# Optimization experiments

Hardware: AMD Instinct MI355X
Metric: run time of the kernel (lower is better)

The kernel has to match this reference:

```python
import jax, jax.numpy as jnp
import numpy as np

N_NODES = 200000
FEAT_DIM = 256
EMB_DIM = 64
N_EXP = 100000
N_TARGETS = 1024
MAX_CAND = 128


def setup_inputs() -> dict:
    key = jax.random.key(0)
    ks = jax.random.split(key, 10)
    return {
        "x": jax.random.normal(ks[0], (N_NODES, FEAT_DIM), jnp.float32),
        "h": jax.random.normal(ks[1], (N_NODES, EMB_DIM), jnp.float32),
        "degree": jax.random.uniform(ks[2], (N_NODES,), jnp.float32),
        "beta": jax.random.uniform(ks[3], (N_NODES,), jnp.float32),
        "exp_nodes": jax.random.randint(ks[4], (N_EXP,), 0, N_NODES),
        "idx_targets": jax.random.randint(ks[5], (N_TARGETS,), 0, N_NODES),
        "W_raw": jax.random.normal(ks[6], (FEAT_DIM, EMB_DIM), jnp.float32) / np.float32(np.sqrt(FEAT_DIM)),
        "b_raw": jnp.zeros((EMB_DIM,), jnp.float32),
        "W_num": jax.random.normal(ks[7], (2, EMB_DIM), jnp.float32),
        "b_num": jnp.zeros((EMB_DIM,), jnp.float32),
        "W1": jax.random.normal(ks[8], (4 * EMB_DIM, EMB_DIM), jnp.float32) / np.float32(np.sqrt(4 * EMB_DIM)),
        "b1": jnp.zeros((EMB_DIM,), jnp.float32),
        "W2": jax.random.normal(ks[9], (EMB_DIM, 1), jnp.float32) / np.float32(np.sqrt(EMB_DIM)),
        "b2": jnp.zeros((1,), jnp.float32),
        "temperature": jnp.float32(1.0),
        "epsilon": jnp.float32(1.0),
    }


def reference(x, h, degree, beta, exp_nodes, idx_targets,
              W_raw, b_raw, W_num, b_num, W1, b1, W2, b2,
              temperature, epsilon):
    # gather node features and project (irregular gather + small GEMM)
    x_v = x[exp_nodes] @ W_raw + b_raw                       # [E, emb]
    h_v = h[exp_nodes]                                       # [E, emb]
    h_T = jnp.broadcast_to(h[idx_targets].mean(axis=0)[None, :],
                           (exp_nodes.shape[0], EMB_DIM))    # [E, emb]
    numerics = jnp.stack([degree[exp_nodes], beta[exp_nodes]], axis=-1)  # [E, 2]
    emb_num = numerics @ W_num + b_num                       # [E, emb]
    emb = jax.nn.relu(jnp.concatenate([x_v, h_v, h_T, emb_num], axis=-1))  # [E, 4*emb]
    # dropout is identity in eval mode
    hidden = jax.nn.relu(emb @ W1 + b1)                      # [E, emb]
    scores = (hidden @ W2 + b2)[:, 0]                        # [E]
    # straight-through gumbel top-k (eval: no gumbel noise, epsilon unused)
    y = jax.nn.softmax(scores / temperature)
    _, idx = jax.lax.top_k(y, MAX_CAND)
    y_hard = jnp.zeros_like(y).at[idx].set(1.0)
    y_st = jax.lax.stop_gradient(y_hard - y) + y
    candidates = y_st[idx]                                   # [MAX_CAND] (== 1.0 fwd)
    cand_indices = exp_nodes[idx]                            # [MAX_CAND]
    return candidates, cand_indices
```

## Files before the change

kernel.cpp:

```cpp
#include <hip/hip_runtime.h>
#include <stdint.h>

#define RELU(v) ((v) > 0.0f ? (v) : 0.0f)

typedef unsigned long long u64;
typedef unsigned int u32;
typedef unsigned short u16;
typedef float f32x4 __attribute__((ext_vector_type(4)));
typedef short bf16x8 __attribute__((ext_vector_type(8)));

constexpr int FEAT = 256;
constexpr int EMB  = 64;

constexpr int STG_ROW = 264;
constexpr int WAVE_BYTES = 16 * STG_ROW * 2;
constexpr int XV_ROW = 68;

__device__ inline u16 bf16_trunc(float v) { return (u16)(__float_as_uint(v) >> 16); }

__device__ inline u32 score_key(float s) {
    u32 u = __float_as_uint(s);
    return (u & 0x80000000u) ? ~u : (u | 0x80000000u);
}

__device__ inline bf16x8 pack_bf16x8(float4 lo, float4 hi) {
    bf16x8 r;
    r[0] = (short)bf16_trunc(lo.x); r[1] = (short)bf16_trunc(lo.y);
    r[2] = (short)bf16_trunc(lo.z); r[3] = (short)bf16_trunc(lo.w);
    r[4] = (short)bf16_trunc(hi.x); r[5] = (short)bf16_trunc(hi.y);
    r[6] = (short)bf16_trunc(hi.z); r[7] = (short)bf16_trunc(hi.w);
    return r;
}

__global__ __launch_bounds__(1024) void setup_kernel(
    const float* __restrict__ h, const int* __restrict__ idx_targets, int nT,
    const float* __restrict__ W_raw, const float* __restrict__ W1, const float* __restrict__ b1,
    float* __restrict__ bias_eff, u16* __restrict__ wrawpk, u16* __restrict__ w1pk)
{
    const int tid = threadIdx.x;
    if (blockIdx.x == 1) {
        for (int t = tid; t < 2048; t += 1024) {
            int ks   = t >> 8;
            int c    = (t >> 6) & 3;
            int lane = t & 63;
            int n    = c * 16 + (lane & 15);
            int kbase = ks * 32 + ((lane >> 4) << 3);
            #pragma unroll
            for (int j = 0; j < 8; ++j) {
                int k = kbase + j;
                wrawpk[t * 8 + j] = bf16_trunc(W_raw[(size_t)k * EMB + n]);
                w1pk  [t * 8 + j] = bf16_trunc(W1   [(size_t)k * EMB + n]);
            }
        }
        return;
    }
    __shared__ int   idx_s[1024];
    __shared__ float partial[16][64];
    __shared__ float hT[64];
    const int nid = nT > 1024 ? 1024 : nT;
    for (int i = tid; i < nid; i += 1024) idx_s[i] = idx_targets[i];
    __syncthreads();
    const int d = tid & 63, grp = tid >> 6;
    float s = 0.f;
    for (int t = grp; t < nid; t += 16)
        s += h[(size_t)idx_s[t] * EMB + d];
    partial[grp][d] = s;
    __syncthreads();
    if (tid < 64) {
        float m = 0.f;
        #pragma unroll
        for (int g = 0; g < 16; ++g) m += partial[g][tid];
        hT[tid] = RELU(m / (float)nT);
    }
    __syncthreads();
    if (tid < 64) {
        float acc = b1[tid];
        #pragma unroll 8
        for (int dd = 0; dd < 64; ++dd)
            acc = fmaf(hT[dd], W1[(size_t)(128 + dd) * EMB + tid], acc);
        bias_eff[tid] = acc;
    }
}

__global__ __launch_bounds__(256) void approx_score_kernel(
    const float* __restrict__ x, const float* __restrict__ h,
    const float* __restrict__ degree, const float* __restrict__ beta,
    const int* __restrict__ exp_nodes,
    const u16* __restrict__ wrawpk, const u16* __restrict__ w1pk,
    const float* __restrict__ b_raw,
    const float* __restrict__ W_num, const float* __restrict__ b_num,
    const float* __restrict__ W2, const float* __restrict__ bias_eff,
    u64* __restrict__ pairs, int E)
{
    __shared__ __align__(16) unsigned char smem[4][WAVE_BYTES];

    const int tid  = threadIdx.x;
    const int wid  = tid >> 6;
    const int lane = tid & 63;
    const int rloc = lane & 15;
    const int kgrp = lane >> 4;
    const int koff = kgrp * 8;
    const int tileBase = blockIdx.x * 64;

    const int grow = tileBase + wid * 16 + rloc;
    const int node = exp_nodes[grow < E ? grow : 0];
    const float* hrow = h + (size_t)node * EMB;
    const float dg = degree[node];
    const float bt = beta[node];

    u16*   stg = (u16*)&smem[wid][0];
    float* xvp = (float*)&smem[wid][0];

    #pragma unroll
    for (int half = 0; half < 2; ++half) {
        float4 v0, v1, v2, v3, v4, v5, v6, v7;
        {
            int r = half * 8;
            v0 = *reinterpret_cast<const float4*>(x + (size_t)__shfl(node, r + 0) * FEAT + lane * 4);
            v1 = *reinterpret_cast<const float4*>(x + (size_t)__shfl(node, r + 1) * FEAT + lane * 4);
            v2 = *reinterpret_cast<const float4*>(x + (size_t)__shfl(node, r + 2) * FEAT + lane * 4);
            v3 = *reinterpret_cast<const float4*>(x + (size_t)__shfl(node, r + 3) * FEAT + lane * 4);
            v4 = *reinterpret_cast<const float4*>(x + (size_t)__shfl(node, r + 4) * FEAT + lane * 4);
            v5 = *reinterpret_cast<const float4*>(x + (size_t)__shfl(node, r + 5) * FEAT + lane * 4);
            v6 = *reinterpret_cast<const float4*>(x + (size_t)__shfl(node, r + 6) * FEAT + lane * 4);
            v7 = *reinterpret_cast<const float4*>(x + (size_t)__shfl(node, r + 7) * FEAT + lane * 4);
        }
        #define STG_WRITE(rr, vv) { \
            ushort4 pk; pk.x = bf16_trunc(vv.x); pk.y = bf16_trunc(vv.y); \
            pk.z = bf16_trunc(vv.z); pk.w = bf16_trunc(vv.w); \
            *reinterpret_cast<ushort4*>(stg + (half * 8 + rr) * STG_ROW + lane * 4) = pk; }
        STG_WRITE(0, v0) STG_WRITE(1, v1) STG_WRITE(2, v2) STG_WRITE(3, v3)
        STG_WRITE(4, v4) STG_WRITE(5, v5) STG_WRITE(6, v6) STG_WRITE(7, v7)
        #undef STG_WRITE
    }
    __builtin_amdgcn_wave_barrier();

    f32x4 acc1[4];
    #pragma unroll
    for (int c = 0; c < 4; ++c) {
        float bv = b_raw[c * 16 + rloc];
        acc1[c] = (f32x4){bv, bv, bv, bv};
    }
    #pragma unroll
    for (int ks = 0; ks < 8; ++ks) {
        bf16x8 a = *reinterpret_cast<const bf16x8*>(stg + rloc * STG_ROW + ks * 32 + koff);
        #pragma unroll
        for (int c = 0; c < 4; ++c) {
            bf16x8 b = *reinterpret_cast<const bf16x8*>(wrawpk + (size_t)((ks * 4 + c) * 64 + lane) * 8);
            acc1[c] = __builtin_amdgcn_mfma_f32_16x16x32_bf16(a, b, acc1[c], 0, 0, 0);
        }
    }
    __builtin_amdgcn_wave_barrier();

    #pragma unroll
    for (int c = 0; c < 4; ++c)
        #pragma unroll
        for (int r = 0; r < 4; ++r)
            xvp[(kgrp * 4 + r) * XV_ROW + c * 16 + rloc] = RELU(acc1[c][r]);
    __builtin_amdgcn_wave_barrier();

    f32x4 acc2[4];
    #pragma unroll
    for (int c = 0; c < 4; ++c) {
        float bv = bias_eff[c * 16 + rloc];
        acc2[c] = (f32x4){bv, bv, bv, bv};
    }

    #pragma unroll
    for (int ks = 0; ks < 2; ++ks) {
        float4 lo = *reinterpret_cast<const float4*>(hrow + ks * 32 + koff);
        float4 hi = *reinterpret_cast<const float4*>(hrow + ks * 32 + koff + 4);
        lo.x = RELU(lo.x); lo.y = RELU(lo.y); lo.z = RELU(lo.z); lo.w = RELU(lo.w);
        hi.x = RELU(hi.x); hi.y = RELU(hi.y); hi.z = RELU(hi.z); hi.w = RELU(hi.w);
        bf16x8 a = pack_bf16x8(lo, hi);
        #pragma unroll
        for (int c = 0; c < 4; ++c) {
            bf16x8 b = *reinterpret_cast<const bf16x8*>(w1pk + (size_t)(((2 + ks) * 4 + c) * 64 + lane) * 8);
            acc2[c] = __builtin_amdgcn_mfma_f32_16x16x32_bf16(a, b, acc2[c], 0, 0, 0);
        }
    }

    #pragma unroll
    for (int ks = 0; ks < 2; ++ks) {
        bf16x8 a;
        #pragma unroll
        for (int j = 0; j < 8; ++j) {
            int k = ks * 32 + koff + j;
            float v = RELU(fmaf(dg, W_num[k], fmaf(bt, W_num[EMB + k], b_num[k])));
            a[j] = (short)bf16_trunc(v);
        }
        #pragma unroll
        for (int c = 0; c < 4; ++c) {
            bf16x8 b = *reinterpret_cast<const bf16x8*>(w1pk + (size_t)(((6 + ks) * 4 + c) * 64 + lane) * 8);
            acc2[c] = __builtin_amdgcn_mfma_f32_16x16x32_bf16(a, b, acc2[c], 0, 0, 0);
        }
    }

    #pragma unroll
    for (int ks = 0; ks < 2; ++ks) {
        float4 lo = *reinterpret_cast<const float4*>(xvp + rloc * XV_ROW + ks * 32 + koff);
        float4 hi = *reinterpret_cast<const float4*>(xvp + rloc * XV_ROW + ks * 32 + koff + 4);
        bf16x8 a = pack_bf16x8(lo, hi);
        #pragma unroll
        for (int c = 0; c < 4; ++c) {
            bf16x8 b = *reinterpret_cast<const bf16x8*>(w1pk + (size_t)((ks * 4 + c) * 64 + lane) * 8);
            acc2[c] = __builtin_amdgcn_mfma_f32_16x16x32_bf16(a, b, acc2[c], 0, 0, 0);
        }
    }

    float p[4] = {0.f, 0.f, 0.f, 0.f};
    #pragma unroll
    for (int c = 0; c < 4; ++c) {
        float w2v = W2[c * 16 + rloc];
        #pragma unroll
        for (int r = 0; r < 4; ++r)
            p[r] = fmaf(RELU(acc2[c][r]), w2v, p[r]);
    }
    #pragma unroll
    for (int m = 1; m < 16; m <<= 1) {
        p[0] += __shfl_xor(p[0], m);
        p[1] += __shfl_xor(p[1], m);
        p[2] += __shfl_xor(p[2], m);
        p[3] += __shfl_xor(p[3], m);
    }
    if (rloc == 0) {
        #pragma unroll
        for (int r = 0; r < 4; ++r) {
            int g = tileBase + wid * 16 + kgrp * 4 + r;
            if (g < E)
                pairs[g] = ((u64)score_key(p[r]) << 32) | (u32)(~(u32)g);
        }
    }
}

template<int N, int NT>
__device__ inline void bitonic_desc(u64* s, int tid) {
    for (int k = 2; k <= N; k <<= 1) {
        for (int j = k >> 1; j > 0; j >>= 1) {
            __syncthreads();
            for (int i = tid; i < N; i += NT) {
                int ixj = i ^ j;
                if (ixj > i) {
                    u64 a = s[i], b = s[ixj];
                    bool sw = ((i & k) == 0) ? (a < b) : (a > b);
                    if (sw) { s[i] = b; s[ixj] = a; }
                }
            }
        }
    }
    __syncthreads();
}

template<int N, int NT, int KEEP>
__global__ __launch_bounds__(NT) void seg_sort_kernel(
    const u64* __restrict__ in, int n_in, int seg, u64* __restrict__ out)
{
    __shared__ u64 s[N];
    int tid = threadIdx.x;
    int base = blockIdx.x * seg;
    for (int i = tid; i < N; i += NT) {
        int g = base + i;
        s[i] = (i < seg && g < n_in) ? in[g] : 0ULL;
    }
    bitonic_desc<N, NT>(s, tid);
    if (tid < KEEP) out[blockIdx.x * KEEP + tid] = s[tid];
}

__global__ __launch_bounds__(256) void rescore_kernel(
    const float* __restrict__ x, const float* __restrict__ h,
    const float* __restrict__ degree, const float* __restrict__ beta,
    const int* __restrict__ exp_nodes,
    const float* __restrict__ W_raw, const float* __restrict__ b_raw,
    const float* __restrict__ W_num, const float* __restrict__ b_num,
    const float* __restrict__ W1, const float* __restrict__ W2,
    const float* __restrict__ bias_eff,
    const u64* __restrict__ cand, u64* __restrict__ pairs2, int E)
{
    __shared__ float emb[4][192];
    const int tid = threadIdx.x;
    const int wid = tid >> 6;
    const int c   = tid & 63;
    const int i   = blockIdx.x * 4 + wid;

    const u64 raw = cand[i];
    const u32 low = (u32)raw;
    const u32 ge  = ~low;
    const int node = (raw != 0ULL && ge < (u32)E) ? exp_nodes[ge] : 0;

    const float* xrow = x + (size_t)node * FEAT;

    float s0 = b_raw[c], s1 = 0.f, s2 = 0.f, s3 = 0.f;
    for (int k = 0; k < FEAT; k += 4) {
        s0 = fmaf(xrow[k + 0], W_raw[(size_t)(k + 0) * EMB + c], s0);
        s1 = fmaf(xrow[k + 1], W_raw[(size_t)(k + 1) * EMB + c], s1);
        s2 = fmaf(xrow[k + 2], W_raw[(size_t)(k + 2) * EMB + c], s2);
        s3 = fmaf(xrow[k + 3], W_raw[(size_t)(k + 3) * EMB + c], s3);
    }
    float xv = (s0 + s1) + (s2 + s3);

    emb[wid][c]       = RELU(xv);
    emb[wid][64 + c]  = RELU(h[(size_t)node * EMB + c]);
    emb[wid][128 + c] = RELU(fmaf(degree[node], W_num[c], fmaf(beta[node], W_num[EMB + c], b_num[c])));
    __syncthreads();

    float h0 = bias_eff[c], h1 = 0.f, h2 = 0.f, h3 = 0.f;
    for (int j = 0; j < 64; j += 2) {
        h0 = fmaf(emb[wid][j],     W1[(size_t)j * EMB + c],       h0);
        h1 = fmaf(emb[wid][j + 1], W1[(size_t)(j + 1) * EMB + c], h1);
    }
    for (int j = 0; j < 64; j += 2) {
        h2 = fmaf(emb[wid][64 + j],     W1[(size_t)(64 + j) * EMB + c],     h2);
        h3 = fmaf(emb[wid][64 + j + 1], W1[(size_t)(64 + j + 1) * EMB + c], h3);
    }
    for (int j = 0; j < 64; j += 2) {
        h0 = fmaf(emb[wid][128 + j],     W1[(size_t)(192 + j) * EMB + c],     h0);
        h1 = fmaf(emb[wid][128 + j + 1], W1[(size_t)(192 + j + 1) * EMB + c], h1);
    }
    float hid = (h0 + h1) + (h2 + h3);

    float p = RELU(hid) * W2[c];
    #pragma unroll
    for (int m = 1; m < 64; m <<= 1) p += __shfl_xor(p, m);

    if (c == 0)
        pairs2[i] = (raw == 0ULL) ? 0ULL : (((u64)score_key(p) << 32) | low);
}

__global__ __launch_bounds__(1024) void topk_final_kernel(
    const u64* __restrict__ in,
    const int* __restrict__ exp_nodes, float* __restrict__ out)
{
    __shared__ u64 s[1024];
    int tid = threadIdx.x;
    s[tid] = in[tid];
    bitonic_desc<1024, 1024>(s, tid);
    if (tid < 128) {
        u64 p = s[tid];
        u32 idx = ~(u32)(p & 0xFFFFFFFFu);
        out[tid]       = 1.0f;
        out[128 + tid] = (float)exp_nodes[idx];
    }
}

extern "C" void kernel_launch(void* const* d_in, const int* in_sizes, int n_in,
                              void* d_out, int out_size, void* d_ws, size_t ws_size,
                              hipStream_t stream) {
    const float* x          = (const float*)d_in[0];
    const float* h          = (const float*)d_in[1];
    const float* degree     = (const float*)d_in[2];
    const float* beta       = (const float*)d_in[3];
    const int*   exp_nodes  = (const int*)d_in[4];
    const int*   idx_targets= (const int*)d_in[5];
    const float* W_raw      = (const float*)d_in[6];
    const float* b_raw      = (const float*)d_in[7];
    const float* W_num      = (const float*)d_in[8];
    const float* b_num      = (const float*)d_in[9];
    const float* W1         = (const float*)d_in[10];
    const float* b1         = (const float*)d_in[11];
    const float* W2         = (const float*)d_in[12];

    int E  = in_sizes[4];
    int nT = in_sizes[5];

    char* ws = (char*)d_ws;
    float* bias_eff = (float*)ws;
    u16* wrawpk = (u16*)(ws + 256);
    u16* w1pk   = (u16*)(ws + 256 + 32768);
    u64* pairs  = (u64*)(ws + 256 + 65536);
    size_t pairs_bytes = (((size_t)E * 8) + 255) / 256 * 256;
    u64* cand1  = (u64*)(ws + 256 + 65536 + pairs_bytes);
    u64* cand2  = (u64*)(ws + 256 + 65536 + pairs_bytes + 262144);
    u64* pairs2 = (u64*)(ws + 256 + 65536 + pairs_bytes + 262144 + 8192);

    setup_kernel<<<2, 1024, 0, stream>>>(h, idx_targets, nT, W_raw, W1, b1,
                                         bias_eff, wrawpk, w1pk);

    int nTiles = (E + 63) / 64;
    approx_score_kernel<<<nTiles, 256, 0, stream>>>(x, h, degree, beta, exp_nodes,
                                                    wrawpk, w1pk, b_raw, W_num, b_num,
                                                    W2, bias_eff, pairs, E);

    int seg1 = (E + 127) / 128;
    seg_sort_kernel<1024, 512, 256><<<128, 512, 0, stream>>>(pairs, E, seg1, cand1);

    seg_sort_kernel<1024, 512, 32><<<32, 512, 0, stream>>>(cand1, 32768, 1024, cand2);

    rescore_kernel<<<256, 256, 0, stream>>>(x, h, degree, beta, exp_nodes,
                                            W_raw, b_raw, W_num, b_num, W1, W2,
                                            bias_eff, cand2, pairs2, E);

    topk_final_kernel<<<1, 1024, 0, stream>>>(pairs2, exp_nodes, (float*)d_out);
}
```

Before: 127.8 us.

## Switch approximate scoring to 32x32x16 MFMA with 32-row tiles per wave

Each wave of the approximate scoring kernel now covers 32 rows instead of 16 and uses the 32x32x16 bf16 MFMA in place of the 16x16x32 one. The weight packing in the setup kernel is rearranged to match the new operand layout, and blocks shrink to 128 threads with a 2-blocks-per-CU launch bound. The goal is fewer MFMA issues and fewer weight loads per row, at the price of larger accumulators, more registers, a longer shuffle reduction over 16 values, and changed LDS padding that could bring bank conflicts.

```diff
diff --git a/kernel.cpp b/kernel.cpp
--- a/kernel.cpp
+++ b/kernel.cpp
@@ -6,15 +6,15 @@
 typedef unsigned long long u64;
 typedef unsigned int u32;
 typedef unsigned short u16;
-typedef float f32x4 __attribute__((ext_vector_type(4)));
+typedef float f32x16 __attribute__((ext_vector_type(16)));
 typedef short bf16x8 __attribute__((ext_vector_type(8)));
 
 constexpr int FEAT = 256;
 constexpr int EMB  = 64;
 
-constexpr int STG_ROW = 264;
-constexpr int WAVE_BYTES = 16 * STG_ROW * 2;
-constexpr int XV_ROW = 68;
+constexpr int STG_ROW = 260;
+constexpr int WAVE_BYTES = 32 * STG_ROW * 2;
+constexpr int XV_ROW = 66;
 
 __device__ inline u16 bf16_trunc(float v) { return (u16)(__float_as_uint(v) >> 16); }
 
@@ -39,17 +39,29 @@
 {
     const int tid = threadIdx.x;
     if (blockIdx.x == 1) {
-        for (int t = tid; t < 2048; t += 1024) {
-            int ks   = t >> 8;
-            int c    = (t >> 6) & 3;
-            int lane = t & 63;
-            int n    = c * 16 + (lane & 15);
-            int kbase = ks * 32 + ((lane >> 4) << 3);
-            #pragma unroll
-            for (int j = 0; j < 8; ++j) {
-                int k = kbase + j;
-                wrawpk[t * 8 + j] = bf16_trunc(W_raw[(size_t)k * EMB + n]);
-                w1pk  [t * 8 + j] = bf16_trunc(W1   [(size_t)k * EMB + n]);
+        for (int i = tid; i < 56 * 64; i += 1024) {
+            int tup  = i >> 6;
+            int lane = i & 63;
+            int n32  = lane & 31;
+            int koff = (lane >> 5) * 8;
+            if (tup < 32) {
+                int ks = tup >> 1, c = tup & 1;
+                int n = c * 32 + n32;
+                #pragma unroll
+                for (int j = 0; j < 8; ++j) {
+                    int k = ks * 16 + koff + j;
+                    wrawpk[(size_t)i * 8 + j] = bf16_trunc(W_raw[(size_t)k * EMB + n]);
+                }
+            } else {
+                int tt = tup - 32;
+                int b = tt >> 3, ks = (tt >> 1) & 3, c = tt & 1;
+                int base = (b == 0) ? 0 : (b == 1 ? 64 : 192);
+                int n = c * 32 + n32;
+                #pragma unroll
+                for (int j = 0; j < 8; ++j) {
+                    int k = base + ks * 16 + koff + j;
+                    w1pk[(size_t)(i - 32 * 64) * 8 + j] = bf16_trunc(W1[(size_t)k * EMB + n]);
+                }
             }
         }
         return;
@@ -82,7 +94,7 @@
     }
 }
 
-__global__ __launch_bounds__(256) void approx_score_kernel(
+__global__ __launch_bounds__(128, 2) void approx_score_kernel(
     const float* __restrict__ x, const float* __restrict__ h,
     const float* __restrict__ degree, const float* __restrict__ beta,
     const int* __restrict__ exp_nodes,
@@ -92,17 +104,16 @@
     const float* __restrict__ W2, const float* __restrict__ bias_eff,
     u64* __restrict__ pairs, int E)
 {
-    __shared__ __align__(16) unsigned char smem[4][WAVE_BYTES];
-
-    const int tid  = threadIdx.x;
-    const int wid  = tid >> 6;
-    const int lane = tid & 63;
-    const int rloc = lane & 15;
-    const int kgrp = lane >> 4;
-    const int koff = kgrp * 8;
+    __shared__ __align__(16) unsigned char smem[2][WAVE_BYTES];
+
+    const int tid   = threadIdx.x;
+    const int wid   = tid >> 6;
+    const int lane  = tid & 63;
+    const int row32 = lane & 31;
+    const int kh    = lane >> 5;
     const int tileBase = blockIdx.x * 64;
 
-    const int grow = tileBase + wid * 16 + rloc;
+    const int grow = tileBase + wid * 32 + row32;
     const int node = exp_nodes[grow < E ? grow : 0];
     const float* hrow = h + (size_t)node * EMB;
     const float dg = degree[node];
@@ -112,10 +123,10 @@
     float* xvp = (float*)&smem[wid][0];
 
     #pragma unroll
-    for (int half = 0; half < 2; ++half) {
+    for (int bch = 0; bch < 4; ++bch) {
         float4 v0, v1, v2, v3, v4, v5, v6, v7;
         {
-            int r = half * 8;
+            int r = bch * 8;
             v0 = *reinterpret_cast<const float4*>(x + (size_t)__shfl(node, r + 0) * FEAT + lane * 4);
             v1 = *reinterpret_cast<const float4*>(x + (size_t)__shfl(node, r + 1) * FEAT + lane * 4);
             v2 = *reinterpret_cast<const float4*>(x + (size_t)__shfl(node, r + 2) * FEAT + lane * 4);
@@ -128,105 +139,107 @@
         #define STG_WRITE(rr, vv) { \
             ushort4 pk; pk.x = bf16_trunc(vv.x); pk.y = bf16_trunc(vv.y); \
             pk.z = bf16_trunc(vv.z); pk.w = bf16_trunc(vv.w); \
-            *reinterpret_cast<ushort4*>(stg + (half * 8 + rr) * STG_ROW + lane * 4) = pk; }
+            *reinterpret_cast<ushort4*>(stg + (bch * 8 + rr) * STG_ROW + lane * 4) = pk; }
         STG_WRITE(0, v0) STG_WRITE(1, v1) STG_WRITE(2, v2) STG_WRITE(3, v3)
         STG_WRITE(4, v4) STG_WRITE(5, v5) STG_WRITE(6, v6) STG_WRITE(7, v7)
         #undef STG_WRITE
     }
     __builtin_amdgcn_wave_barrier();
 
-    f32x4 acc1[4];
-    #pragma unroll
-    for (int c = 0; c < 4; ++c) {
-        float bv = b_raw[c * 16 + rloc];
-        acc1[c] = (f32x4){bv, bv, bv, bv};
-    }
-    #pragma unroll
-    for (int ks = 0; ks < 8; ++ks) {
-        bf16x8 a = *reinterpret_cast<const bf16x8*>(stg + rloc * STG_ROW + ks * 32 + koff);
-        #pragma unroll
-        for (int c = 0; c < 4; ++c) {
-            bf16x8 b = *reinterpret_cast<const bf16x8*>(wrawpk + (size_t)((ks * 4 + c) * 64 + lane) * 8);
-            acc1[c] = __builtin_amdgcn_mfma_f32_16x16x32_bf16(a, b, acc1[c], 0, 0, 0);
+    f32x16 acc1[2];
+    #pragma unroll
+    for (int c = 0; c < 2; ++c) {
+        float bv = b_raw[c * 32 + row32];
+        #pragma unroll
+        for (int r = 0; r < 16; ++r) acc1[c][r] = bv;
+    }
+    #pragma unroll
+    for (int ks = 0; ks < 16; ++ks) {
+        bf16x8 a = *reinterpret_cast<const bf16x8*>(stg + row32 * STG_ROW + ks * 16 + kh * 8);
+        #pragma unroll
+        for (int c = 0; c < 2; ++c) {
+            bf16x8 b = *reinterpret_cast<const bf16x8*>(wrawpk + (size_t)((ks * 2 + c) * 64 + lane) * 8);
+            acc1[c] = __builtin_amdgcn_mfma_f32_32x32x16_bf16(a, b, acc1[c], 0, 0, 0);
         }
     }
     __builtin_amdgcn_wave_barrier();
 
     #pragma unroll
-    for (int c = 0; c < 4; ++c)
-        #pragma unroll
-        for (int r = 0; r < 4; ++r)
-            xvp[(kgrp * 4 + r) * XV_ROW + c * 16 + rloc] = RELU(acc1[c][r]);
+    for (int c = 0; c < 2; ++c)
+        #pragma unroll
+        for (int r = 0; r < 16; ++r) {
+            int row = (r & 3) + 8 * (r >> 2) + 4 * kh;
+            xvp[row * XV_ROW + c * 32 + row32] = RELU(acc1[c][r]);
+        }
     __builtin_amdgcn_wave_barrier();
 
-    f32x4 acc2[4];
-    #pragma unroll
-    for (int c = 0; c < 4; ++c) {
-        float bv = bias_eff[c * 16 + rloc];
-        acc2[c] = (f32x4){bv, bv, bv, bv};
-    }
-
-    #pragma unroll
-    for (int ks = 0; ks < 2; ++ks) {
-        float4 lo = *reinterpret_cast<const float4*>(hrow + ks * 32 + koff);
-        float4 hi = *reinterpret_cast<const float4*>(hrow + ks * 32 + koff + 4);
+    f32x16 acc2[2];
+    #pragma unroll
+    for (int c = 0; c < 2; ++c) {
+        float bv = bias_eff[c * 32 + row32];
+        #pragma unroll
+        for (int r = 0; r < 16; ++r) acc2[c][r] = bv;
+    }
+
+    #pragma unroll
+    for (int ks = 0; ks < 4; ++ks) {
+        const float* xp = xvp + row32 * XV_ROW + ks * 16 + kh * 8;
+        float4 lo = *reinterpret_cast<const float4*>(xp);
+        float4 hi = *reinterpret_cast<const float4*>(xp + 4);
+        bf16x8 a = pack_bf16x8(lo, hi);
+        #pragma unroll
+        for (int c = 0; c < 2; ++c) {
+            bf16x8 b = *reinterpret_cast<const bf16x8*>(w1pk + (size_t)((ks * 2 + c) * 64 + lane) * 8);
+            acc2[c] = __builtin_amdgcn_mfma_f32_32x32x16_bf16(a, b, acc2[c], 0, 0, 0);
+        }
+    }
+
+    #pragma unroll
+    for (int ks = 0; ks < 4; ++ks) {
+        const float* hp = hrow + ks * 16 + kh * 8;
+        float4 lo = *reinterpret_cast<const float4*>(hp);
+        float4 hi = *reinterpret_cast<const float4*>(hp + 4);
         lo.x = RELU(lo.x); lo.y = RELU(lo.y); lo.z = RELU(lo.z); lo.w = RELU(lo.w);
         hi.x = RELU(hi.x); hi.y = RELU(hi.y); hi.z = RELU(hi.z); hi.w = RELU(hi.w);
         bf16x8 a = pack_bf16x8(lo, hi);
         #pragma unroll
-        for (int c = 0; c < 4; ++c) {
-            bf16x8 b = *reinterpret_cast<const bf16x8*>(w1pk + (size_t)(((2 + ks) * 4 + c) * 64 + lane) * 8);
-            acc2[c] = __builtin_amdgcn_mfma_f32_16x16x32_bf16(a, b, acc2[c], 0, 0, 0);
-        }
-    }
-
-    #pragma unroll
-    for (int ks = 0; ks < 2; ++ks) {
+        for (int c = 0; c < 2; ++c) {
+            bf16x8 b = *reinterpret_cast<const bf16x8*>(w1pk + (size_t)((8 + ks * 2 + c) * 64 + lane) * 8);
+            acc2[c] = __builtin_amdgcn_mfma_f32_32x32x16_bf16(a, b, acc2[c], 0, 0, 0);
+        }
+    }
+
+    #pragma unroll
+    for (int ks = 0; ks < 4; ++ks) {
         bf16x8 a;
         #pragma unroll
         for (int j = 0; j < 8; ++j) {
-            int k = ks * 32 + koff + j;
+            int k = ks * 16 + kh * 8 + j;
             float v = RELU(fmaf(dg, W_num[k], fmaf(bt, W_num[EMB + k], b_num[k])));
             a[j] = (short)bf16_trunc(v);
         }
         #pragma unroll
-        for (int c = 0; c < 4; ++c) {
-            bf16x8 b = *reinterpret_cast<const bf16x8*>(w1pk + (size_t)(((6 + ks) * 4 + c) * 64 + lane) * 8);
-            acc2[c] = __builtin_amdgcn_mfma_f32_16x16x32_bf16(a, b, acc2[c], 0, 0, 0);
-        }
-    }
-
-    #pragma unroll
-    for (int ks = 0; ks < 2; ++ks) {
-        float4 lo = *reinterpret_cast<const float4*>(xvp + rloc * XV_ROW + ks * 32 + koff);
-        float4 hi = *reinterpret_cast<const float4*>(xvp + rloc * XV_ROW + ks * 32 + koff + 4);
-        bf16x8 a = pack_bf16x8(lo, hi);
-        #pragma unroll
-        for (int c = 0; c < 4; ++c) {
-            bf16x8 b = *reinterpret_cast<const bf16x8*>(w1pk + (size_t)((ks * 4 + c) * 64 + lane) * 8);
-            acc2[c] = __builtin_amdgcn_mfma_f32_16x16x32_bf16(a, b, acc2[c], 0, 0, 0);
-        }
-    }
-
-    float p[4] = {0.f, 0.f, 0.f, 0.f};
-    #pragma unroll
-    for (int c = 0; c < 4; ++c) {
-        float w2v = W2[c * 16 + rloc];
-        #pragma unroll
-        for (int r = 0; r < 4; ++r)
-            p[r] = fmaf(RELU(acc2[c][r]), w2v, p[r]);
-    }
-    #pragma unroll
-    for (int m = 1; m < 16; m <<= 1) {
-        p[0] += __shfl_xor(p[0], m);
-        p[1] += __shfl_xor(p[1], m);
-        p[2] += __shfl_xor(p[2], m);
-        p[3] += __shfl_xor(p[3], m);
-    }
-    if (rloc == 0) {
-        #pragma unroll
-        for (int r = 0; r < 4; ++r) {
-            int g = tileBase + wid * 16 + kgrp * 4 + r;
+        for (int c = 0; c < 2; ++c) {
+            bf16x8 b = *reinterpret_cast<const bf16x8*>(w1pk + (size_t)((16 + ks * 2 + c) * 64 + lane) * 8);
+            acc2[c] = __builtin_amdgcn_mfma_f32_32x32x16_bf16(a, b, acc2[c], 0, 0, 0);
+        }
+    }
+
+    float w2a = W2[row32], w2b = W2[32 + row32];
+    float p[16];
+    #pragma unroll
+    for (int r = 0; r < 16; ++r)
+        p[r] = RELU(acc2[0][r]) * w2a + RELU(acc2[1][r]) * w2b;
+    #pragma unroll
+    for (int m = 1; m < 32; m <<= 1) {
+        #pragma unroll
+        for (int r = 0; r < 16; ++r) p[r] += __shfl_xor(p[r], m);
+    }
+    if (row32 == 0) {
+        #pragma unroll
+        for (int r = 0; r < 16; ++r) {
+            int row = (r & 3) + 8 * (r >> 2) + 4 * kh;
+            int g = tileBase + wid * 32 + row;
             if (g < E)
                 pairs[g] = ((u64)score_key(p[r]) << 32) | (u32)(~(u32)g);
         }
@@ -376,7 +389,7 @@
                                          bias_eff, wrawpk, w1pk);
 
     int nTiles = (E + 63) / 64;
-    approx_score_kernel<<<nTiles, 256, 0, stream>>>(x, h, degree, beta, exp_nodes,
+    approx_score_kernel<<<nTiles, 128, 0, stream>>>(x, h, degree, beta, exp_nodes,
                                                     wrawpk, w1pk, b_raw, W_num, b_num,
                                                     W2, bias_eff, pairs, E);
 
```

Result: slower. 133.7 us (+4.6%).

## Fuse sort, rescore and final top-k stages into one cooperative kernel

Applied to the files above, without the earlier changes.

Replaces four small back-to-back launches (two segmented bitonic sorts, the exact rescore, the final top-k sort) with a single cooperative kernel of 128 blocks that uses grid-wide syncs between stages. This targets per-launch overhead and the gaps between tiny kernels at the tail of the pipeline. Rescoring now runs 8 candidates per block with a wave barrier instead of a block barrier, and the final sort uses 512 threads instead of 1024. Grid syncs have their own cost, and cooperative launch requires all blocks to be co-resident.

```diff
diff --git a/kernel.cpp b/kernel.cpp
--- a/kernel.cpp
+++ b/kernel.cpp
@@ -1,5 +1,8 @@
 #include <hip/hip_runtime.h>
+#include <hip/hip_cooperative_groups.h>
 #include <stdint.h>
+
+namespace cg = cooperative_groups;
 
 #define RELU(v) ((v) > 0.0f ? (v) : 0.0f)
 
@@ -251,22 +254,9 @@
     __syncthreads();
 }
 
-template<int N, int NT, int KEEP>
-__global__ __launch_bounds__(NT) void seg_sort_kernel(
-    const u64* __restrict__ in, int n_in, int seg, u64* __restrict__ out)
-{
-    __shared__ u64 s[N];
-    int tid = threadIdx.x;
-    int base = blockIdx.x * seg;
-    for (int i = tid; i < N; i += NT) {
-        int g = base + i;
-        s[i] = (i < seg && g < n_in) ? in[g] : 0ULL;
-    }
-    bitonic_desc<N, NT>(s, tid);
-    if (tid < KEEP) out[blockIdx.x * KEEP + tid] = s[tid];
-}
-
-__global__ __launch_bounds__(256) void rescore_kernel(
+__global__ __launch_bounds__(512) void chain_kernel(
+    const u64* __restrict__ pairs, int E, int seg1,
+    u64* __restrict__ cand1, u64* __restrict__ cand2, u64* __restrict__ pairs2,
     const float* __restrict__ x, const float* __restrict__ h,
     const float* __restrict__ degree, const float* __restrict__ beta,
     const int* __restrict__ exp_nodes,
@@ -274,71 +264,93 @@
     const float* __restrict__ W_num, const float* __restrict__ b_num,
     const float* __restrict__ W1, const float* __restrict__ W2,
     const float* __restrict__ bias_eff,
-    const u64* __restrict__ cand, u64* __restrict__ pairs2, int E)
+    float* __restrict__ out)
 {
-    __shared__ float emb[4][192];
+    cg::grid_group grid = cg::this_grid();
+    __shared__ u64  s[1024];
+    __shared__ float emb[8][192];
+
     const int tid = threadIdx.x;
-    const int wid = tid >> 6;
-    const int c   = tid & 63;
-    const int i   = blockIdx.x * 4 + wid;
-
-    const u64 raw = cand[i];
-    const u32 low = (u32)raw;
-    const u32 ge  = ~low;
-    const int node = (raw != 0ULL && ge < (u32)E) ? exp_nodes[ge] : 0;
-
-    const float* xrow = x + (size_t)node * FEAT;
-
-    float s0 = b_raw[c], s1 = 0.f, s2 = 0.f, s3 = 0.f;
-    for (int k = 0; k < FEAT; k += 4) {
-        s0 = fmaf(xrow[k + 0], W_raw[(size_t)(k + 0) * EMB + c], s0);
-        s1 = fmaf(xrow[k + 1], W_raw[(size_t)(k + 1) * EMB + c], s1);
-        s2 = fmaf(xrow[k + 2], W_raw[(size_t)(k + 2) * EMB + c], s2);
-        s3 = fmaf(xrow[k + 3], W_raw[(size_t)(k + 3) * EMB + c], s3);
-    }
-    float xv = (s0 + s1) + (s2 + s3);
-
-    emb[wid][c]       = RELU(xv);
-    emb[wid][64 + c]  = RELU(h[(size_t)node * EMB + c]);
-    emb[wid][128 + c] = RELU(fmaf(degree[node], W_num[c], fmaf(beta[node], W_num[EMB + c], b_num[c])));
-    __syncthreads();
-
-    float h0 = bias_eff[c], h1 = 0.f, h2 = 0.f, h3 = 0.f;
-    for (int j = 0; j < 64; j += 2) {
-        h0 = fmaf(emb[wid][j],     W1[(size_t)j * EMB + c],       h0);
-        h1 = fmaf(emb[wid][j + 1], W1[(size_t)(j + 1) * EMB + c], h1);
-    }
-    for (int j = 0; j < 64; j += 2) {
-        h2 = fmaf(emb[wid][64 + j],     W1[(size_t)(64 + j) * EMB + c],     h2);
-        h3 = fmaf(emb[wid][64 + j + 1], W1[(size_t)(64 + j + 1) * EMB + c], h3);
-    }
-    for (int j = 0; j < 64; j += 2) {
-        h0 = fmaf(emb[wid][128 + j],     W1[(size_t)(192 + j) * EMB + c],     h0);
-        h1 = fmaf(emb[wid][128 + j + 1], W1[(size_t)(192 + j + 1) * EMB + c], h1);
-    }
-    float hid = (h0 + h1) + (h2 + h3);
-
-    float p = RELU(hid) * W2[c];
-    #pragma unroll
-    for (int m = 1; m < 64; m <<= 1) p += __shfl_xor(p, m);
-
-    if (c == 0)
-        pairs2[i] = (raw == 0ULL) ? 0ULL : (((u64)score_key(p) << 32) | low);
-}
-
-__global__ __launch_bounds__(1024) void topk_final_kernel(
-    const u64* __restrict__ in,
-    const int* __restrict__ exp_nodes, float* __restrict__ out)
-{
-    __shared__ u64 s[1024];
-    int tid = threadIdx.x;
-    s[tid] = in[tid];
-    bitonic_desc<1024, 1024>(s, tid);
-    if (tid < 128) {
-        u64 p = s[tid];
-        u32 idx = ~(u32)(p & 0xFFFFFFFFu);
-        out[tid]       = 1.0f;
-        out[128 + tid] = (float)exp_nodes[idx];
+    const int bid = blockIdx.x;
+
+    {
+        int base = bid * seg1;
+        for (int i = tid; i < 1024; i += 512) {
+            int g = base + i;
+            s[i] = (i < seg1 && g < E) ? pairs[g] : 0ULL;
+        }
+        bitonic_desc<1024, 512>(s, tid);
+        if (tid < 256) cand1[bid * 256 + tid] = s[tid];
+    }
+    grid.sync();
+
+    if (bid < 32) {
+        for (int i = tid; i < 1024; i += 512)
+            s[i] = cand1[bid * 1024 + i];
+        bitonic_desc<1024, 512>(s, tid);
+        if (tid < 32) cand2[bid * 32 + tid] = s[tid];
+    }
+    grid.sync();
+
+    {
+        const int wid = tid >> 6;
+        const int c   = tid & 63;
+        const int i   = bid * 8 + wid;
+
+        const u64 raw = cand2[i];
+        const u32 low = (u32)raw;
+        const u32 ge  = ~low;
+        const int node = (raw != 0ULL && ge < (u32)E) ? exp_nodes[ge] : 0;
+
+        const float* xrow = x + (size_t)node * FEAT;
+
+        float s0 = b_raw[c], s1 = 0.f, s2 = 0.f, s3 = 0.f;
+        for (int k = 0; k < FEAT; k += 4) {
+            s0 = fmaf(xrow[k + 0], W_raw[(size_t)(k + 0) * EMB + c], s0);
+            s1 = fmaf(xrow[k + 1], W_raw[(size_t)(k + 1) * EMB + c], s1);
+            s2 = fmaf(xrow[k + 2], W_raw[(size_t)(k + 2) * EMB + c], s2);
+            s3 = fmaf(xrow[k + 3], W_raw[(size_t)(k + 3) * EMB + c], s3);
+        }
+        float xv = (s0 + s1) + (s2 + s3);
+
+        emb[wid][c]       = RELU(xv);
+        emb[wid][64 + c]  = RELU(h[(size_t)node * EMB + c]);
+        emb[wid][128 + c] = RELU(fmaf(degree[node], W_num[c], fmaf(beta[node], W_num[EMB + c], b_num[c])));
+        __builtin_amdgcn_wave_barrier();
+
+        float h0 = bias_eff[c], h1 = 0.f, h2 = 0.f, h3 = 0.f;
+        for (int j = 0; j < 64; j += 2) {
+            h0 = fmaf(emb[wid][j],     W1[(size_t)j * EMB + c],       h0);
+            h1 = fmaf(emb[wid][j + 1], W1[(size_t)(j + 1) * EMB + c], h1);
+        }
+        for (int j = 0; j < 64; j += 2) {
+            h2 = fmaf(emb[wid][64 + j],     W1[(size_t)(64 + j) * EMB + c],     h2);
+            h3 = fmaf(emb[wid][64 + j + 1], W1[(size_t)(64 + j + 1) * EMB + c], h3);
+        }
+        for (int j = 0; j < 64; j += 2) {
+            h0 = fmaf(emb[wid][128 + j],     W1[(size_t)(192 + j) * EMB + c],     h0);
+            h1 = fmaf(emb[wid][128 + j + 1], W1[(size_t)(192 + j + 1) * EMB + c], h1);
+        }
+        float hid = (h0 + h1) + (h2 + h3);
+
+        float p = RELU(hid) * W2[c];
+        #pragma unroll
+        for (int m = 1; m < 64; m <<= 1) p += __shfl_xor(p, m);
+
+        if (c == 0)
+            pairs2[i] = (raw == 0ULL) ? 0ULL : (((u64)score_key(p) << 32) | low);
+    }
+    grid.sync();
+
+    if (bid == 0) {
+        for (int i = tid; i < 1024; i += 512) s[i] = pairs2[i];
+        bitonic_desc<1024, 512>(s, tid);
+        if (tid < 128) {
+            u64 p = s[tid];
+            u32 idx = ~(u32)(p & 0xFFFFFFFFu);
+            out[tid]       = 1.0f;
+            out[128 + tid] = (float)exp_nodes[idx];
+        }
     }
 }
 
@@ -371,6 +383,7 @@
     u64* cand1  = (u64*)(ws + 256 + 65536 + pairs_bytes);
     u64* cand2  = (u64*)(ws + 256 + 65536 + pairs_bytes + 262144);
     u64* pairs2 = (u64*)(ws + 256 + 65536 + pairs_bytes + 262144 + 8192);
+    float* outf = (float*)d_out;
 
     setup_kernel<<<2, 1024, 0, stream>>>(h, idx_targets, nT, W_raw, W1, b1,
                                          bias_eff, wrawpk, w1pk);
@@ -381,13 +394,13 @@
                                                     W2, bias_eff, pairs, E);
 
     int seg1 = (E + 127) / 128;
-    seg_sort_kernel<1024, 512, 256><<<128, 512, 0, stream>>>(pairs, E, seg1, cand1);
-
-    seg_sort_kernel<1024, 512, 32><<<32, 512, 0, stream>>>(cand1, 32768, 1024, cand2);
-
-    rescore_kernel<<<256, 256, 0, stream>>>(x, h, degree, beta, exp_nodes,
-                                            W_raw, b_raw, W_num, b_num, W1, W2,
-                                            bias_eff, cand2, pairs2, E);
-
-    topk_final_kernel<<<1, 1024, 0, stream>>>(pairs2, exp_nodes, (float*)d_out);
-}
+    void* args[] = {
+        (void*)&pairs, (void*)&E, (void*)&seg1,
+        (void*)&cand1, (void*)&cand2, (void*)&pairs2,
+        (void*)&x, (void*)&h, (void*)&degree, (void*)&beta, (void*)&exp_nodes,
+        (void*)&W_raw, (void*)&b_raw, (void*)&W_num, (void*)&b_num,
+        (void*)&W1, (void*)&W2, (void*)&bias_eff, (void*)&outf
+    };
+    hipLaunchCooperativeKernel((void*)chain_kernel, dim3(128), dim3(512),
+                               args, 0, stream);
+}
```

Measured after the change: 183.1 us. 1.43x slower.

## Fuse per-block top-12 selection into scoring kernel and drop a sort stage

Applied to the files above, without the earlier changes.

Each 64-row scoring block now runs a wave-level bitonic sort of its scores in registers and writes only its top 12 candidates, in place of writing all scores to a full pairs array. This removes the first segmented sort pass and the large pairs buffer write. The remaining single segmented sort keeps 52 per 1024-element segment, which sets the rescore grid and final top-k input size. The cost is an extra block barrier and shuffle sort in the scoring kernel, plus the risk of dropping true top-128 candidates if more than 12 fall in one block or more than 52 in one segment.

```diff
diff --git a/kernel.cpp b/kernel.cpp
--- a/kernel.cpp
+++ b/kernel.cpp
@@ -15,6 +15,7 @@
 constexpr int STG_ROW = 264;
 constexpr int WAVE_BYTES = 16 * STG_ROW * 2;
 constexpr int XV_ROW = 68;
+constexpr int KEEP_BLK = 12;
 
 __device__ inline u16 bf16_trunc(float v) { return (u16)(__float_as_uint(v) >> 16); }
 
@@ -90,9 +91,10 @@
     const float* __restrict__ b_raw,
     const float* __restrict__ W_num, const float* __restrict__ b_num,
     const float* __restrict__ W2, const float* __restrict__ bias_eff,
-    u64* __restrict__ pairs, int E)
+    u64* __restrict__ cand1, int E)
 {
     __shared__ __align__(16) unsigned char smem[4][WAVE_BYTES];
+    __shared__ u64 sarr[64];
 
     const int tid  = threadIdx.x;
     const int wid  = tid >> 6;
@@ -226,10 +228,26 @@
     if (rloc == 0) {
         #pragma unroll
         for (int r = 0; r < 4; ++r) {
-            int g = tileBase + wid * 16 + kgrp * 4 + r;
-            if (g < E)
-                pairs[g] = ((u64)score_key(p[r]) << 32) | (u32)(~(u32)g);
-        }
+            int lrow = wid * 16 + kgrp * 4 + r;
+            int g = tileBase + lrow;
+            sarr[lrow] = (g < E) ? (((u64)score_key(p[r]) << 32) | (u32)(~(u32)g)) : 0ULL;
+        }
+    }
+    __syncthreads();
+
+    if (wid == 0) {
+        u64 v = sarr[lane];
+        #pragma unroll
+        for (int k = 2; k <= 64; k <<= 1) {
+            #pragma unroll
+            for (int j = k >> 1; j > 0; j >>= 1) {
+                u64 o = __shfl_xor(v, j);
+                bool lower = (lane & j) == 0;
+                bool dir   = (lane & k) == 0;
+                v = (lower == dir) ? (v > o ? v : o) : (v < o ? v : o);
+            }
+        }
+        if (lane < KEEP_BLK) cand1[(size_t)blockIdx.x * KEEP_BLK + lane] = v;
     }
 }
 
@@ -327,12 +345,12 @@
 }
 
 __global__ __launch_bounds__(1024) void topk_final_kernel(
-    const u64* __restrict__ in,
+    const u64* __restrict__ in, int n_in,
     const int* __restrict__ exp_nodes, float* __restrict__ out)
 {
     __shared__ u64 s[1024];
     int tid = threadIdx.x;
-    s[tid] = in[tid];
+    s[tid] = (tid < n_in) ? in[tid] : 0ULL;
     bitonic_desc<1024, 1024>(s, tid);
     if (tid < 128) {
         u64 p = s[tid];
@@ -362,32 +380,32 @@
     int E  = in_sizes[4];
     int nT = in_sizes[5];
 
+    int nTiles = (E + 63) / 64;
+    int nCand1 = nTiles * KEEP_BLK;
+    int nSel   = (nCand1 + 1023) / 1024;
+    int nKept  = nSel * 52;
+    int nResc  = (nKept + 3) / 4;
+
     char* ws = (char*)d_ws;
     float* bias_eff = (float*)ws;
     u16* wrawpk = (u16*)(ws + 256);
     u16* w1pk   = (u16*)(ws + 256 + 32768);
-    u64* pairs  = (u64*)(ws + 256 + 65536);
-    size_t pairs_bytes = (((size_t)E * 8) + 255) / 256 * 256;
-    u64* cand1  = (u64*)(ws + 256 + 65536 + pairs_bytes);
-    u64* cand2  = (u64*)(ws + 256 + 65536 + pairs_bytes + 262144);
-    u64* pairs2 = (u64*)(ws + 256 + 65536 + pairs_bytes + 262144 + 8192);
+    u64* cand1  = (u64*)(ws + 256 + 65536);
+    u64* cand2  = (u64*)(ws + 256 + 65536 + 163840);
+    u64* pairs2 = (u64*)(ws + 256 + 65536 + 163840 + 8192);
 
     setup_kernel<<<2, 1024, 0, stream>>>(h, idx_targets, nT, W_raw, W1, b1,
                                          bias_eff, wrawpk, w1pk);
 
-    int nTiles = (E + 63) / 64;
     approx_score_kernel<<<nTiles, 256, 0, stream>>>(x, h, degree, beta, exp_nodes,
                                                     wrawpk, w1pk, b_raw, W_num, b_num,
-                                                    W2, bias_eff, pairs, E);
-
-    int seg1 = (E + 127) / 128;
-    seg_sort_kernel<1024, 512, 256><<<128, 512, 0, stream>>>(pairs, E, seg1, cand1);
-
-    seg_sort_kernel<1024, 512, 32><<<32, 512, 0, stream>>>(cand1, 32768, 1024, cand2);
-
-    rescore_kernel<<<256, 256, 0, stream>>>(x, h, degree, beta, exp_nodes,
-                                            W_raw, b_raw, W_num, b_num, W1, W2,
-                                            bias_eff, cand2, pairs2, E);
-
-    topk_final_kernel<<<1, 1024, 0, stream>>>(pairs2, exp_nodes, (float*)d_out);
-}
+                                                    W2, bias_eff, cand1, E);
+
+    seg_sort_kernel<1024, 512, 52><<<nSel, 512, 0, stream>>>(cand1, nCand1, 1024, cand2);
+
+    rescore_kernel<<<nResc, 256, 0, stream>>>(x, h, degree, beta, exp_nodes,
+                                              W_raw, b_raw, W_num, b_num, W1, W2,
+                                              bias_eff, cand2, pairs2, E);
+
+    topk_final_kernel<<<1, 1024, 0, stream>>>(pairs2, nKept, exp_nodes, (float*)d_out);
+}
```

Measured after the change: 107.8 us. 1.19x faster.
